# Optimization experiments

Hardware: AMD Instinct MI355X
Metric: run time of the kernel (lower is better)

Reference implementation:

```python
import jax, jax.numpy as jnp
import numpy as np

ITERATIONS = 4


def setup_inputs() -> dict:
    key = jax.random.key(0)
    x = jax.random.normal(key, (256, 512, 256), dtype=jnp.float32)
    return {"x": x}


def reference(x):
    # axis == 1 branch of the torch module (default)
    N, len_m, len_d = x.shape
    m = jnp.mean(x, axis=1, keepdims=True)          # [N, 1, D]
    xn = x - m                                      # [N, M, D]
    # sigma = xn^T xn / (M - 1)  -> [N, D, D]
    sigma = jnp.einsum('nmd,nme->nde', xn, xn) / (len_m - 1)

    # trace-normalized Newton-Schulz iteration for inverse sqrt
    trace = jnp.trace(sigma, axis1=-2, axis2=-1)[:, None, None]  # [N, 1, 1]
    sigma_norm = sigma / trace
    P = jnp.broadcast_to(jnp.eye(len_d, dtype=x.dtype), (N, len_d, len_d))
    for _ in range(ITERATIONS):
        P3 = P @ P @ P                              # matrix_power(P, 3), batched
        P = 1.5 * P - 0.5 * (P3 @ sigma_norm)
    wm = P / jnp.sqrt(trace)                        # whitening matrix [N, D, D]

    decorrelated = xn @ wm                          # [N, M, D]
    return decorrelated
```

## Files before the change

### kernel.cpp

```cpp
#include <hip/hip_runtime.h>
#include <stdint.h>

#define Nn 256
#define Mm 512
#define Dd 256

typedef unsigned short u16;
typedef unsigned int u32;
typedef __attribute__((ext_vector_type(8))) short bf16x8;
typedef __attribute__((ext_vector_type(4))) float f32x4;

__device__ __forceinline__ u16 f2b(float f) {
    unsigned u = __float_as_uint(f);
    return (u16)((u + 0x7FFFu + ((u >> 16) & 1u)) >> 16);
}
__device__ __forceinline__ float b2f(u16 h) {
    return __uint_as_float(((unsigned)h) << 16);
}
__device__ __forceinline__ void glds16(const u16* g, u16* l) {
    __builtin_amdgcn_global_load_lds((const __attribute__((address_space(1))) void*)g,
                                     (__attribute__((address_space(3))) void*)l, 16, 0, 0);
}

__global__ __launch_bounds__(256) void mean_part_kernel(const float* __restrict__ x,
                                                        float* __restrict__ meanPart) {
    const int bid = blockIdx.x;
    const int n = bid >> 2, c = bid & 3;
    const int tid = threadIdx.x;
    const float* xb = x + (size_t)n * Mm * Dd + (size_t)c * 128 * Dd;
    float a0 = 0.f, a1 = 0.f, a2 = 0.f, a3 = 0.f;
    for (int m = 0; m < 128; m += 4) {
        a0 += xb[(m + 0) * Dd + tid];
        a1 += xb[(m + 1) * Dd + tid];
        a2 += xb[(m + 2) * Dd + tid];
        a3 += xb[(m + 3) * Dd + tid];
    }
    meanPart[((size_t)n * 4 + c) * Dd + tid] = a0 + a1 + a2 + a3;
}

__global__ __launch_bounds__(256) void center_tr_kernel(const float* __restrict__ x,
                                                        const float* __restrict__ meanPart,
                                                        u16* __restrict__ xn,
                                                        u16* __restrict__ xnT) {
    __shared__ float meanS[Dd];
    __shared__ u16 tileS[64 * 66];
    const int bid = blockIdx.x;
    const int n = bid >> 3, mt = bid & 7;
    const int tid = threadIdx.x;

    const float* mp = meanPart + (size_t)n * 4 * Dd;
    meanS[tid] = (mp[tid] + mp[Dd + tid] + mp[2 * Dd + tid] + mp[3 * Dd + tid]) * (1.0f / Mm);
    __syncthreads();

    const float* xb = x + (size_t)n * Mm * Dd;
    u16* xnb = xn + (size_t)n * Mm * Dd;
    u16* xtb = xnT + (size_t)n * Dd * Mm;
    const int mrow = tid >> 4, dq = tid & 15;
    const int tx2 = (tid & 31) * 2, ty = tid >> 5;

    for (int dt = 0; dt < Dd / 64; ++dt) {
        #pragma unroll
        for (int rr = 0; rr < 4; ++rr) {
            int ml = mrow + 16 * rr;
            int m = mt * 64 + ml;
            int d = dt * 64 + dq * 4;
            float4 v = *(const float4*)(xb + (size_t)m * Dd + d);
            float4 mu = *(const float4*)(meanS + d);
            u16 b0 = f2b(v.x - mu.x), b1 = f2b(v.y - mu.y);
            u16 b2 = f2b(v.z - mu.z), b3 = f2b(v.w - mu.w);
            u32 lo = (u32)b0 | ((u32)b1 << 16);
            u32 hi = (u32)b2 | ((u32)b3 << 16);
            *(uint2*)(xnb + (size_t)m * Dd + d) = make_uint2(lo, hi);
            tileS[(dq * 4 + 0) * 66 + ml] = b0;
            tileS[(dq * 4 + 1) * 66 + ml] = b1;
            tileS[(dq * 4 + 2) * 66 + ml] = b2;
            tileS[(dq * 4 + 3) * 66 + ml] = b3;
        }
        __syncthreads();
        #pragma unroll
        for (int r = 0; r < 8; ++r) {
            int dl = r * 8 + ty;
            u32 w = *(const u32*)(tileS + dl * 66 + tx2);
            *(u32*)(xtb + (size_t)(dt * 64 + dl) * Mm + mt * 64 + tx2) = w;
        }
        __syncthreads();
    }
}

__global__ __launch_bounds__(256) void sigma_kernel(const u16* __restrict__ xnT,
                                                    float* __restrict__ sigma) {
    __shared__ u16 sA[128 * 32];
    __shared__ u16 sB[128 * 32];
    const int bid = blockIdx.x;
    const int xcd = bid & 7, slot = bid >> 3;
    const int t = slot & 3;
    const int n = ((slot >> 2) << 3) | xcd;
    const int tr = t >> 1, tc = t & 1;
    const int tid = threadIdx.x;
    const int lane = tid & 63, wave = tid >> 6;
    const int wr = wave >> 1, wc = wave & 1;
    const int l15 = lane & 15, quad = lane >> 4;
    const int row0 = tid >> 2, q = tid & 3;
    const int wb8 = (tid & 192) * 8;

    const u16* base = xnT + (size_t)n * Dd * Mm;
    const u16* gA = base + (size_t)(tr * 128) * Mm;
    const u16* gB = base + (size_t)(tc * 128) * Mm;

    f32x4 acc[4][4];
    #pragma unroll
    for (int i = 0; i < 4; ++i)
        #pragma unroll
        for (int j = 0; j < 4; ++j) acc[i][j] = (f32x4){0.f, 0.f, 0.f, 0.f};

    for (int kk = 0; kk < Mm; kk += 32) {
        glds16(gA + (size_t)row0 * Mm + kk + q * 8, sA + wb8);
        glds16(gA + (size_t)(row0 + 64) * Mm + kk + q * 8, sA + 2048 + wb8);
        glds16(gB + (size_t)row0 * Mm + kk + q * 8, sB + wb8);
        glds16(gB + (size_t)(row0 + 64) * Mm + kk + q * 8, sB + 2048 + wb8);
        __syncthreads();
        bf16x8 a[4], b[4];
        #pragma unroll
        for (int i = 0; i < 4; ++i) a[i] = *(const bf16x8*)(sA + (wr * 64 + i * 16 + l15) * 32 + quad * 8);
        #pragma unroll
        for (int j = 0; j < 4; ++j) b[j] = *(const bf16x8*)(sB + (wc * 64 + j * 16 + l15) * 32 + quad * 8);
        #pragma unroll
        for (int i = 0; i < 4; ++i)
            #pragma unroll
            for (int j = 0; j < 4; ++j)
                acc[i][j] = __builtin_amdgcn_mfma_f32_16x16x32_bf16(a[i], b[j], acc[i][j], 0, 0, 0);
        __syncthreads();
    }

    float* sg = sigma + (size_t)n * Dd * Dd;
    #pragma unroll
    for (int i = 0; i < 4; ++i)
        #pragma unroll
        for (int j = 0; j < 4; ++j)
            #pragma unroll
            for (int r = 0; r < 4; ++r) {
                int row = tr * 128 + wr * 64 + i * 16 + quad * 4 + r;
                int col = tc * 128 + wc * 64 + j * 16 + l15;
                sg[row * Dd + col] = acc[i][j][r];
            }
}

__global__ __launch_bounds__(256) void normalize_kernel(const float* __restrict__ sigma,
                                                        u16* __restrict__ Sh, u16* __restrict__ Sl,
                                                        u16* __restrict__ P,
                                                        float* __restrict__ rtr) {
    __shared__ float red[256];
    const int n = blockIdx.x, tid = threadIdx.x;
    const float* sg = sigma + (size_t)n * Dd * Dd;
    red[tid] = sg[tid * (Dd + 1)];
    __syncthreads();
    for (int s = 128; s > 0; s >>= 1) {
        if (tid < s) red[tid] += red[tid + s];
        __syncthreads();
    }
    const float raw = red[0];
    const float inv = 1.0f / raw;
    if (tid == 0) rtr[n] = sqrtf(511.0f * inv);

    const size_t mb = (size_t)n * Dd * Dd;
    for (int r = 0; r < Dd; ++r) {
        size_t idx = mb + (size_t)r * Dd + tid;
        float s = sg[r * Dd + tid] * inv;
        u16 sh = f2b(s);
        Sh[idx] = sh;
        Sl[idx] = f2b(s - b2f(sh));
        P[idx] = f2b(((r == tid) ? 1.5f : 0.0f) - 0.5f * s);
    }
}

__global__ __launch_bounds__(256) void ns_gemm(const u16* __restrict__ A,
                                               const u16* __restrict__ Bh, const u16* __restrict__ Bl,
                                               u16* __restrict__ outH,
                                               const float* __restrict__ rtr, int mode, int bsplit) {
    __shared__ u16 sA[128 * 32], sBh[128 * 32], sBl[128 * 32];
    const int bid = blockIdx.x;
    const int xcd = bid & 7, slot = bid >> 3;
    const int t = slot & 3;
    const int n = ((slot >> 2) << 3) | xcd;
    const int tr = t >> 1, tc = t & 1;
    const int tid = threadIdx.x;
    const int lane = tid & 63, wave = tid >> 6;
    const int wr = wave >> 1, wc = wave & 1;
    const int l15 = lane & 15, quad = lane >> 4;
    const int row0 = tid >> 2, q = tid & 3;
    const int wb8 = (tid & 192) * 8;

    const size_t mb = (size_t)n * Dd * Dd;
    const u16* gA = A + mb + (size_t)(tr * 128) * Dd;
    const u16* gBh = Bh + mb + (size_t)(tc * 128) * Dd;
    const u16* gBl = Bl + mb + (size_t)(tc * 128) * Dd;

    f32x4 acc[4][4];
    #pragma unroll
    for (int i = 0; i < 4; ++i)
        #pragma unroll
        for (int j = 0; j < 4; ++j) acc[i][j] = (f32x4){0.f, 0.f, 0.f, 0.f};

    for (int kk = 0; kk < Dd; kk += 32) {
        glds16(gA + (size_t)row0 * Dd + kk + q * 8, sA + wb8);
        glds16(gA + (size_t)(row0 + 64) * Dd + kk + q * 8, sA + 2048 + wb8);
        glds16(gBh + (size_t)row0 * Dd + kk + q * 8, sBh + wb8);
        glds16(gBh + (size_t)(row0 + 64) * Dd + kk + q * 8, sBh + 2048 + wb8);
        if (bsplit) {
            glds16(gBl + (size_t)row0 * Dd + kk + q * 8, sBl + wb8);
            glds16(gBl + (size_t)(row0 + 64) * Dd + kk + q * 8, sBl + 2048 + wb8);
        }
        __syncthreads();
        bf16x8 a[4], bh[4];
        #pragma unroll
        for (int i = 0; i < 4; ++i) a[i] = *(const bf16x8*)(sA + (wr * 64 + i * 16 + l15) * 32 + quad * 8);
        #pragma unroll
        for (int j = 0; j < 4; ++j) bh[j] = *(const bf16x8*)(sBh + (wc * 64 + j * 16 + l15) * 32 + quad * 8);
        #pragma unroll
        for (int i = 0; i < 4; ++i)
            #pragma unroll
            for (int j = 0; j < 4; ++j)
                acc[i][j] = __builtin_amdgcn_mfma_f32_16x16x32_bf16(a[i], bh[j], acc[i][j], 0, 0, 0);
        if (bsplit) {
            bf16x8 bl[4];
            #pragma unroll
            for (int j = 0; j < 4; ++j) bl[j] = *(const bf16x8*)(sBl + (wc * 64 + j * 16 + l15) * 32 + quad * 8);
            #pragma unroll
            for (int i = 0; i < 4; ++i)
                #pragma unroll
                for (int j = 0; j < 4; ++j)
                    acc[i][j] = __builtin_amdgcn_mfma_f32_16x16x32_bf16(a[i], bl[j], acc[i][j], 0, 0, 0);
        }
        __syncthreads();
    }

    const float rs = (mode == 2) ? rtr[n] : 0.f;
    #pragma unroll
    for (int i = 0; i < 4; ++i)
        #pragma unroll
        for (int j = 0; j < 4; ++j)
            #pragma unroll
            for (int r = 0; r < 4; ++r) {
                int row = tr * 128 + wr * 64 + i * 16 + quad * 4 + r;
                int col = tc * 128 + wc * 64 + j * 16 + l15;
                size_t idx = mb + (size_t)row * Dd + col;
                float v = acc[i][j][r];
                float o;
                if (mode == 0) o = v;
                else if (mode == 1) o = ((row == col) ? 1.5f : 0.0f) - 0.5f * v;
                else o = v * rs;
                outH[idx] = f2b(o);
            }
}

__global__ __launch_bounds__(256) void final_gemm(const u16* __restrict__ xn,
                                                  const u16* __restrict__ Wh,
                                                  float* __restrict__ out) {
    __shared__ u16 sA[128 * 32];
    __shared__ u16 sB[128 * 32];
    const int bid = blockIdx.x;
    const int xcd = bid & 7, slot = bid >> 3;
    const int t = slot & 7;
    const int n = ((slot >> 3) << 3) | xcd;
    const int tr = t >> 1, tc = t & 1;
    const int tid = threadIdx.x;
    const int lane = tid & 63, wave = tid >> 6;
    const int wr = wave >> 1, wc = wave & 1;
    const int l15 = lane & 15, quad = lane >> 4;
    const int row0 = tid >> 2, q = tid & 3;
    const int wb8 = (tid & 192) * 8;

    const u16* gA = xn + (size_t)n * Mm * Dd + (size_t)(tr * 128) * Dd;
    const u16* gB = Wh + (size_t)n * Dd * Dd + (size_t)(tc * 128) * Dd;

    f32x4 acc[4][4];
    #pragma unroll
    for (int i = 0; i < 4; ++i)
        #pragma unroll
        for (int j = 0; j < 4; ++j) acc[i][j] = (f32x4){0.f, 0.f, 0.f, 0.f};

    for (int kk = 0; kk < Dd; kk += 32) {
        glds16(gA + (size_t)row0 * Dd + kk + q * 8, sA + wb8);
        glds16(gA + (size_t)(row0 + 64) * Dd + kk + q * 8, sA + 2048 + wb8);
        glds16(gB + (size_t)row0 * Dd + kk + q * 8, sB + wb8);
        glds16(gB + (size_t)(row0 + 64) * Dd + kk + q * 8, sB + 2048 + wb8);
        __syncthreads();
        bf16x8 a[4], b[4];
        #pragma unroll
        for (int i = 0; i < 4; ++i) a[i] = *(const bf16x8*)(sA + (wr * 64 + i * 16 + l15) * 32 + quad * 8);
        #pragma unroll
        for (int j = 0; j < 4; ++j) b[j] = *(const bf16x8*)(sB + (wc * 64 + j * 16 + l15) * 32 + quad * 8);
        #pragma unroll
        for (int i = 0; i < 4; ++i)
            #pragma unroll
            for (int j = 0; j < 4; ++j)
                acc[i][j] = __builtin_amdgcn_mfma_f32_16x16x32_bf16(a[i], b[j], acc[i][j], 0, 0, 0);
        __syncthreads();
    }

    float* ob = out + (size_t)n * Mm * Dd;
    #pragma unroll
    for (int i = 0; i < 4; ++i)
        #pragma unroll
        for (int j = 0; j < 4; ++j)
            #pragma unroll
            for (int r = 0; r < 4; ++r) {
                int row = tr * 128 + wr * 64 + i * 16 + quad * 4 + r;
                int col = tc * 128 + wc * 64 + j * 16 + l15;
                ob[(size_t)row * Dd + col] = acc[i][j][r];
            }
}

extern "C" void kernel_launch(void* const* d_in, const int* in_sizes, int n_in,
                              void* d_out, int out_size, void* d_ws, size_t ws_size,
                              hipStream_t stream) {
    const float* x = (const float*)d_in[0];
    float* out = (float*)d_out;
    char* ws = (char*)d_ws;
    const size_t MB32 = 33554432;

    u16* xn = (u16*)(ws + 0);
    u16* xnT = (u16*)(ws + 2 * MB32);
    u16* P0 = (u16*)(ws + 2 * MB32);
    u16* E = (u16*)(ws + 3 * MB32);
    float* sigma = (float*)(ws + 4 * MB32);
    u16* Q = (u16*)(ws + 4 * MB32);
    u16* P1 = (u16*)(ws + 5 * MB32);
    u16* Sh = (u16*)(ws + 6 * MB32);
    u16* Sl = (u16*)(ws + 7 * MB32);
    float* meanPart = (float*)(ws + 9 * MB32);
    float* rtr = (float*)(ws + 9 * MB32 + 4194304);

    mean_part_kernel<<<Nn * 4, 256, 0, stream>>>(x, meanPart);
    center_tr_kernel<<<Nn * 8, 256, 0, stream>>>(x, meanPart, xn, xnT);
    sigma_kernel<<<Nn * 4, 256, 0, stream>>>(xnT, sigma);
    normalize_kernel<<<Nn, 256, 0, stream>>>(sigma, Sh, Sl, P0, rtr);

    ns_gemm<<<Nn * 4, 256, 0, stream>>>(P0, P0, P0, Q, rtr, 0, 0);
    ns_gemm<<<Nn * 4, 256, 0, stream>>>(Q, Sh, Sl, E, rtr, 1, 1);
    ns_gemm<<<Nn * 4, 256, 0, stream>>>(P0, E, E, P1, rtr, 0, 0);
    ns_gemm<<<Nn * 4, 256, 0, stream>>>(P1, P1, P1, Q, rtr, 0, 0);
    ns_gemm<<<Nn * 4, 256, 0, stream>>>(Q, Sh, Sl, E, rtr, 1, 1);
    ns_gemm<<<Nn * 4, 256, 0, stream>>>(P1, E, E, P0, rtr, 0, 0);
    ns_gemm<<<Nn * 4, 256, 0, stream>>>(P0, P0, P0, Q, rtr, 0, 0);
    ns_gemm<<<Nn * 4, 256, 0, stream>>>(Q, Sh, Sl, E, rtr, 1, 1);
    ns_gemm<<<Nn * 4, 256, 0, stream>>>(P0, E, E, P1, rtr, 2, 0);

    final_gemm<<<Nn * 8, 256, 0, stream>>>(xn, P1, out);
}
```

Before: 625.7 us.

## Fuse normalize and Newton-Schulz GEMM chain into one persistent per-matrix kernel

Replaces the normalize kernel and the nine separate ns_gemm launches with a single kernel. It launches one 1024-thread block per batch matrix and computes full 256x256 GEMMs back to back, with double-buffered 64-wide K panels in an XOR-swizzled LDS layout. This removes launch gaps and the cross-kernel round trips of intermediates, and keeps each matrix's data local to one CU and likely in cache. In exchange it runs only one block per CU, with in-place output writes that rely on block-level synchronisation, and it uses a large LDS footprint that limits occupancy.

```diff
diff --git a/kernel.cpp b/kernel.cpp
--- a/kernel.cpp
+++ b/kernel.cpp
@@ -145,112 +145,141 @@
             }
 }
 
-__global__ __launch_bounds__(256) void normalize_kernel(const float* __restrict__ sigma,
-                                                        u16* __restrict__ Sh, u16* __restrict__ Sl,
-                                                        u16* __restrict__ P,
-                                                        float* __restrict__ rtr) {
-    __shared__ float red[256];
-    const int n = blockIdx.x, tid = threadIdx.x;
-    const float* sg = sigma + (size_t)n * Dd * Dd;
-    red[tid] = sg[tid * (Dd + 1)];
+__device__ __forceinline__ void stage_panel(const u16* __restrict__ g, u16* s, int tid) {
+    const int wv = tid >> 6, l = tid & 63;
+    const int rl = l >> 3;
+    const int gch = (l & 7) ^ rl;
+    u16* base = s + wv * 512;
+    const u16* g0 = g + (size_t)(wv * 8 + rl) * 256 + gch * 8;
+    glds16(g0, base);
+    glds16(g0 + 128 * 256, base + 8192);
+}
+
+__device__ __forceinline__ bf16x8 fragr(const u16* s, int row, int kc) {
+    return *(const bf16x8*)(s + row * 64 + ((kc ^ (row & 7)) << 3));
+}
+
+template<bool SAME, bool SPLIT, int MODE>
+__device__ __forceinline__ void gemm256(const u16* __restrict__ gA,
+                                        const u16* __restrict__ gBh,
+                                        const u16* __restrict__ gBl,
+                                        u16* __restrict__ dst, float rs,
+                                        u16* sbuf, int tid) {
+    const int lane = tid & 63, wave = tid >> 6;
+    const int wr = wave >> 2, wc = wave & 3;
+    const int l15 = lane & 15, quad = lane >> 4;
+
+    f32x4 acc[4][4];
+    #pragma unroll
+    for (int i = 0; i < 4; ++i)
+        #pragma unroll
+        for (int j = 0; j < 4; ++j) acc[i][j] = (f32x4){0.f, 0.f, 0.f, 0.f};
+
+    __syncthreads();
+    constexpr int NP = SPLIT ? 8 : 4;
+    stage_panel(gA, sbuf, tid);
+    if (!SAME) stage_panel(gBh, sbuf + 16384, tid);
+    __syncthreads();
+
+    for (int p = 0; p < NP; ++p) {
+        const int b = p & 1;
+        if (p + 1 < NP) {
+            const int kn = (SPLIT ? ((p + 1) & 3) : (p + 1)) * 64;
+            u16* nb = sbuf + (b ^ 1) * 32768;
+            stage_panel(gA + kn, nb, tid);
+            if (!SAME) {
+                const u16* gsrc = (SPLIT && (p + 1) >= 4) ? gBl : gBh;
+                stage_panel(gsrc + kn, nb + 16384, tid);
+            }
+        }
+        const u16* cA = sbuf + b * 32768;
+        const u16* cB = SAME ? cA : (cA + 16384);
+        #pragma unroll
+        for (int ks = 0; ks < 2; ++ks) {
+            bf16x8 af[4], bfr[4];
+            #pragma unroll
+            for (int i = 0; i < 4; ++i) af[i] = fragr(cA, wr * 64 + i * 16 + l15, ks * 4 + quad);
+            #pragma unroll
+            for (int j = 0; j < 4; ++j) bfr[j] = fragr(cB, wc * 64 + j * 16 + l15, ks * 4 + quad);
+            #pragma unroll
+            for (int i = 0; i < 4; ++i)
+                #pragma unroll
+                for (int j = 0; j < 4; ++j)
+                    acc[i][j] = __builtin_amdgcn_mfma_f32_16x16x32_bf16(af[i], bfr[j], acc[i][j], 0, 0, 0);
+        }
+        __syncthreads();
+    }
+
+    #pragma unroll
+    for (int i = 0; i < 4; ++i)
+        #pragma unroll
+        for (int j = 0; j < 4; ++j)
+            #pragma unroll
+            for (int r = 0; r < 4; ++r) {
+                int row = wr * 64 + i * 16 + quad * 4 + r;
+                int col = wc * 64 + j * 16 + l15;
+                float v = acc[i][j][r];
+                float o;
+                if (MODE == 0) o = v;
+                else if (MODE == 1) o = ((row == col) ? 1.5f : 0.0f) - 0.5f * v;
+                else o = v * rs;
+                dst[row * 256 + col] = f2b(o);
+            }
+}
+
+__global__ __launch_bounds__(1024) void ns_chain_kernel(const float* __restrict__ sigma,
+                                                        u16* __restrict__ PQ,
+                                                        u16* __restrict__ Sh,
+                                                        u16* __restrict__ Sl) {
+    __shared__ u16 sPan[4][16384];
+    float* red = (float*)&sPan[0][0];
+
+    const int n = blockIdx.x;
+    const int tid = threadIdx.x;
+
+    const float* sg = sigma + (size_t)n * 65536;
+    u16* P = PQ + (size_t)n * 131072;
+    u16* QE = P + 65536;
+    u16* shp = Sh + (size_t)n * 65536;
+    u16* slp = Sl + (size_t)n * 65536;
+
+    if (tid < 256) red[tid] = sg[tid * 257];
     __syncthreads();
     for (int s = 128; s > 0; s >>= 1) {
         if (tid < s) red[tid] += red[tid + s];
         __syncthreads();
     }
-    const float raw = red[0];
-    const float inv = 1.0f / raw;
-    if (tid == 0) rtr[n] = sqrtf(511.0f * inv);
-
-    const size_t mb = (size_t)n * Dd * Dd;
-    for (int r = 0; r < Dd; ++r) {
-        size_t idx = mb + (size_t)r * Dd + tid;
-        float s = sg[r * Dd + tid] * inv;
-        u16 sh = f2b(s);
-        Sh[idx] = sh;
-        Sl[idx] = f2b(s - b2f(sh));
-        P[idx] = f2b(((r == tid) ? 1.5f : 0.0f) - 0.5f * s);
-    }
-}
-
-__global__ __launch_bounds__(256) void ns_gemm(const u16* __restrict__ A,
-                                               const u16* __restrict__ Bh, const u16* __restrict__ Bl,
-                                               u16* __restrict__ outH,
-                                               const float* __restrict__ rtr, int mode, int bsplit) {
-    __shared__ u16 sA[128 * 32], sBh[128 * 32], sBl[128 * 32];
-    const int bid = blockIdx.x;
-    const int xcd = bid & 7, slot = bid >> 3;
-    const int t = slot & 3;
-    const int n = ((slot >> 2) << 3) | xcd;
-    const int tr = t >> 1, tc = t & 1;
-    const int tid = threadIdx.x;
-    const int lane = tid & 63, wave = tid >> 6;
-    const int wr = wave >> 1, wc = wave & 1;
-    const int l15 = lane & 15, quad = lane >> 4;
-    const int row0 = tid >> 2, q = tid & 3;
-    const int wb8 = (tid & 192) * 8;
-
-    const size_t mb = (size_t)n * Dd * Dd;
-    const u16* gA = A + mb + (size_t)(tr * 128) * Dd;
-    const u16* gBh = Bh + mb + (size_t)(tc * 128) * Dd;
-    const u16* gBl = Bl + mb + (size_t)(tc * 128) * Dd;
-
-    f32x4 acc[4][4];
-    #pragma unroll
-    for (int i = 0; i < 4; ++i)
-        #pragma unroll
-        for (int j = 0; j < 4; ++j) acc[i][j] = (f32x4){0.f, 0.f, 0.f, 0.f};
-
-    for (int kk = 0; kk < Dd; kk += 32) {
-        glds16(gA + (size_t)row0 * Dd + kk + q * 8, sA + wb8);
-        glds16(gA + (size_t)(row0 + 64) * Dd + kk + q * 8, sA + 2048 + wb8);
-        glds16(gBh + (size_t)row0 * Dd + kk + q * 8, sBh + wb8);
-        glds16(gBh + (size_t)(row0 + 64) * Dd + kk + q * 8, sBh + 2048 + wb8);
-        if (bsplit) {
-            glds16(gBl + (size_t)row0 * Dd + kk + q * 8, sBl + wb8);
-            glds16(gBl + (size_t)(row0 + 64) * Dd + kk + q * 8, sBl + 2048 + wb8);
-        }
-        __syncthreads();
-        bf16x8 a[4], bh[4];
-        #pragma unroll
-        for (int i = 0; i < 4; ++i) a[i] = *(const bf16x8*)(sA + (wr * 64 + i * 16 + l15) * 32 + quad * 8);
-        #pragma unroll
-        for (int j = 0; j < 4; ++j) bh[j] = *(const bf16x8*)(sBh + (wc * 64 + j * 16 + l15) * 32 + quad * 8);
-        #pragma unroll
-        for (int i = 0; i < 4; ++i)
-            #pragma unroll
-            for (int j = 0; j < 4; ++j)
-                acc[i][j] = __builtin_amdgcn_mfma_f32_16x16x32_bf16(a[i], bh[j], acc[i][j], 0, 0, 0);
-        if (bsplit) {
-            bf16x8 bl[4];
-            #pragma unroll
-            for (int j = 0; j < 4; ++j) bl[j] = *(const bf16x8*)(sBl + (wc * 64 + j * 16 + l15) * 32 + quad * 8);
-            #pragma unroll
-            for (int i = 0; i < 4; ++i)
-                #pragma unroll
-                for (int j = 0; j < 4; ++j)
-                    acc[i][j] = __builtin_amdgcn_mfma_f32_16x16x32_bf16(a[i], bl[j], acc[i][j], 0, 0, 0);
-        }
-        __syncthreads();
-    }
-
-    const float rs = (mode == 2) ? rtr[n] : 0.f;
-    #pragma unroll
-    for (int i = 0; i < 4; ++i)
-        #pragma unroll
-        for (int j = 0; j < 4; ++j)
-            #pragma unroll
-            for (int r = 0; r < 4; ++r) {
-                int row = tr * 128 + wr * 64 + i * 16 + quad * 4 + r;
-                int col = tc * 128 + wc * 64 + j * 16 + l15;
-                size_t idx = mb + (size_t)row * Dd + col;
-                float v = acc[i][j][r];
-                float o;
-                if (mode == 0) o = v;
-                else if (mode == 1) o = ((row == col) ? 1.5f : 0.0f) - 0.5f * v;
-                else o = v * rs;
-                outH[idx] = f2b(o);
-            }
+    const float inv = 1.0f / red[0];
+    const float rtr = sqrtf(511.0f * inv);
+
+    #pragma unroll 4
+    for (int it = 0; it < 16; ++it) {
+        int idx = it * 4096 + tid * 4;
+        float4 v = *(const float4*)(sg + idx);
+        int row = idx >> 8, col0 = idx & 255;
+        float s0 = v.x * inv, s1 = v.y * inv, s2 = v.z * inv, s3 = v.w * inv;
+        u16 h0 = f2b(s0), h1 = f2b(s1), h2 = f2b(s2), h3 = f2b(s3);
+        *(uint2*)(shp + idx) = make_uint2((u32)h0 | ((u32)h1 << 16), (u32)h2 | ((u32)h3 << 16));
+        u16 e0 = f2b(s0 - b2f(h0)), e1 = f2b(s1 - b2f(h1));
+        u16 e2 = f2b(s2 - b2f(h2)), e3 = f2b(s3 - b2f(h3));
+        *(uint2*)(slp + idx) = make_uint2((u32)e0 | ((u32)e1 << 16), (u32)e2 | ((u32)e3 << 16));
+        u16 p0 = f2b(((row == col0 + 0) ? 1.5f : 0.f) - 0.5f * s0);
+        u16 p1 = f2b(((row == col0 + 1) ? 1.5f : 0.f) - 0.5f * s1);
+        u16 p2 = f2b(((row == col0 + 2) ? 1.5f : 0.f) - 0.5f * s2);
+        u16 p3 = f2b(((row == col0 + 3) ? 1.5f : 0.f) - 0.5f * s3);
+        *(uint2*)(P + idx) = make_uint2((u32)p0 | ((u32)p1 << 16), (u32)p2 | ((u32)p3 << 16));
+    }
+
+    u16* sbuf = &sPan[0][0];
+    #pragma unroll 1
+    for (int it = 0; it < 3; ++it) {
+        gemm256<true, false, 0>(P, P, (const u16*)nullptr, QE, 0.f, sbuf, tid);
+        gemm256<false, true, 1>(QE, shp, slp, QE, 0.f, sbuf, tid);
+        if (it < 2)
+            gemm256<false, false, 0>(P, QE, (const u16*)nullptr, P, 0.f, sbuf, tid);
+        else
+            gemm256<false, false, 2>(P, QE, (const u16*)nullptr, P, rtr, sbuf, tid);
+    }
 }
 
 __global__ __launch_bounds__(256) void final_gemm(const u16* __restrict__ xn,
@@ -271,7 +300,7 @@
     const int wb8 = (tid & 192) * 8;
 
     const u16* gA = xn + (size_t)n * Mm * Dd + (size_t)(tr * 128) * Dd;
-    const u16* gB = Wh + (size_t)n * Dd * Dd + (size_t)(tc * 128) * Dd;
+    const u16* gB = Wh + (size_t)n * 131072 + (size_t)(tc * 128) * Dd;
 
     f32x4 acc[4][4];
     #pragma unroll
@@ -321,30 +350,15 @@
 
     u16* xn = (u16*)(ws + 0);
     u16* xnT = (u16*)(ws + 2 * MB32);
-    u16* P0 = (u16*)(ws + 2 * MB32);
-    u16* E = (u16*)(ws + 3 * MB32);
+    u16* PQ = (u16*)(ws + 2 * MB32);
     float* sigma = (float*)(ws + 4 * MB32);
-    u16* Q = (u16*)(ws + 4 * MB32);
-    u16* P1 = (u16*)(ws + 5 * MB32);
     u16* Sh = (u16*)(ws + 6 * MB32);
     u16* Sl = (u16*)(ws + 7 * MB32);
     float* meanPart = (float*)(ws + 9 * MB32);
-    float* rtr = (float*)(ws + 9 * MB32 + 4194304);
 
     mean_part_kernel<<<Nn * 4, 256, 0, stream>>>(x, meanPart);
     center_tr_kernel<<<Nn * 8, 256, 0, stream>>>(x, meanPart, xn, xnT);
     sigma_kernel<<<Nn * 4, 256, 0, stream>>>(xnT, sigma);
-    normalize_kernel<<<Nn, 256, 0, stream>>>(sigma, Sh, Sl, P0, rtr);
-
-    ns_gemm<<<Nn * 4, 256, 0, stream>>>(P0, P0, P0, Q, rtr, 0, 0);
-    ns_gemm<<<Nn * 4, 256, 0, stream>>>(Q, Sh, Sl, E, rtr, 1, 1);
-    ns_gemm<<<Nn * 4, 256, 0, stream>>>(P0, E, E, P1, rtr, 0, 0);
-    ns_gemm<<<Nn * 4, 256, 0, stream>>>(P1, P1, P1, Q, rtr, 0, 0);
-    ns_gemm<<<Nn * 4, 256, 0, stream>>>(Q, Sh, Sl, E, rtr, 1, 1);
-    ns_gemm<<<Nn * 4, 256, 0, stream>>>(P1, E, E, P0, rtr, 0, 0);
-    ns_gemm<<<Nn * 4, 256, 0, stream>>>(P0, P0, P0, Q, rtr, 0, 0);
-    ns_gemm<<<Nn * 4, 256, 0, stream>>>(Q, Sh, Sl, E, rtr, 1, 1);
-    ns_gemm<<<Nn * 4, 256, 0, stream>>>(P0, E, E, P1, rtr, 2, 0);
-
-    final_gemm<<<Nn * 8, 256, 0, stream>>>(xn, P1, out);
-}
+    ns_chain_kernel<<<Nn, 1024, 0, stream>>>(sigma, PQ, Sh, Sl);
+    final_gemm<<<Nn * 8, 256, 0, stream>>>(xn, PQ, out);
+}
```

After: 1.039 ms. +66.1%, slower.
